# Performance work log

Hardware: AMD Instinct MI355X
Metric: run time of the kernel (lower is better)

## Reference

```python
import jax, jax.numpy as jnp
import numpy as np

B, L, E, H = 1, 2048, 1024, 16
HW = E // H  # head width = 64
SCALE = HW ** -0.5


def setup_inputs() -> dict:
    key = jax.random.key(0)
    ks = jax.random.split(key, 8)
    x = jax.random.normal(ks[0], (B, L, E), dtype=jnp.float32)
    mask = jax.random.bernoulli(ks[1], 0.9, (B, L))
    mask = mask.at[:, 0].set(True)  # guarantee at least one valid key per batch
    bias = jax.random.normal(ks[2], (B, L, L, H), dtype=jnp.float32)
    # torch nn.Linear stores weight as [out, in]; we keep that convention
    w_proj = jax.random.normal(ks[3], (3 * E, E), dtype=jnp.float32) * (E ** -0.5)
    w_o = jax.random.normal(ks[4], (E, E), dtype=jnp.float32) * (E ** -0.5)
    b_o = jax.random.normal(ks[5], (E,), dtype=jnp.float32) * 0.02
    w_g = jax.random.normal(ks[6], (E, E), dtype=jnp.float32) * (E ** -0.5)
    b_g = jax.random.normal(ks[7], (E,), dtype=jnp.float32) * 0.02
    return {"x": x, "mask": mask, "bias": bias, "w_proj": w_proj,
            "w_o": w_o, "b_o": b_o, "w_g": w_g, "b_g": b_g}


def reference(x, mask, bias, w_proj, w_o, b_o, w_g, b_g):
    # proj -> [B, L, 3E], rearrange '(h c)' with h=H so each head slice holds [q|k|v]
    t = jnp.einsum('ble,fe->blf', x, w_proj)               # [B, L, 3E]
    t = t.reshape(B, L, H, 3 * HW).transpose(0, 2, 1, 3)   # [B, H, L, 3*HW]
    q, k, v = jnp.split(t, 3, axis=-1)                     # each [B, H, L, HW]
    a = jnp.einsum('bhqc,bhkc->bhqk', SCALE * q, k)        # [B, H, L, L]
    a = a + bias.transpose(0, 3, 1, 2)                     # bias: [B,Lq,Lk,H] -> [B,H,Lq,Lk]
    a = jnp.where(mask[:, None, None, :], a, -jnp.inf)
    a = jax.nn.softmax(a, axis=-1)
    y = jnp.einsum('bhqk,bhkc->bqhc', a, v).reshape(B, L, E)
    g = jax.nn.sigmoid(jnp.einsum('ble,fe->blf', x, w_g) + b_g)
    y = g * y
    return jnp.einsum('ble,fe->blf', y, w_o) + b_o
```

## Files before the change

kernel.cpp:

```cpp
#include <hip/hip_runtime.h>
#include <stdint.h>

#define LSEQ 2048
#define EMB  1024
#define NH   16
#define HWID 64
#define SCALEF 0.125f

typedef __attribute__((ext_vector_type(4))) float  f32x4;
typedef __attribute__((ext_vector_type(8))) short  bf16x8;
typedef __attribute__((ext_vector_type(8))) unsigned short u16x8;
typedef __attribute__((ext_vector_type(4))) unsigned short u16x4;

static __device__ __forceinline__ unsigned short f2bf(float f) {
    union { float f; unsigned int u; } v; v.f = f;
    unsigned int r = (v.u + 0x7FFFu + ((v.u >> 16) & 1u)) >> 16;
    return (unsigned short)r;
}
static __device__ __forceinline__ float bf2f(unsigned short h) {
    union { unsigned int u; float f; } v; v.u = ((unsigned int)h) << 16;
    return v.f;
}

static __device__ __forceinline__ void gload_lds16(const void* g, void* l) {
    __builtin_amdgcn_global_load_lds((const __attribute__((address_space(1))) void*)g,
                                     (__attribute__((address_space(3))) void*)l,
                                     16, 0, 0);
}

__global__ __launch_bounds__(256) void convert_kernel(
    const float* __restrict__ x, const float* __restrict__ wp,
    const float* __restrict__ wg, const float* __restrict__ wo,
    unsigned short* __restrict__ xb, unsigned short* __restrict__ wcat,
    unsigned short* __restrict__ wob)
{
    const int NX  = (LSEQ * EMB) / 4;
    const int NWP = (3 * EMB * EMB) / 4;
    const int NWG = (EMB * EMB) / 4;
    const int NWO = (EMB * EMB) / 4;
    const int total = NX + NWP + NWG + NWO;
    for (int i = blockIdx.x * blockDim.x + threadIdx.x; i < total;
         i += gridDim.x * blockDim.x) {
        const float4* src; unsigned short* dst; int j;
        if (i < NX)                  { src = (const float4*)x;  dst = xb;                  j = i; }
        else if (i < NX + NWP)       { src = (const float4*)wp; dst = wcat;                j = i - NX; }
        else if (i < NX + NWP + NWG) { src = (const float4*)wg; dst = wcat + 3 * EMB * EMB; j = i - NX - NWP; }
        else                         { src = (const float4*)wo; dst = wob;                 j = i - NX - NWP - NWG; }
        float4 v = src[j];
        u16x4 o;
        o.x = f2bf(v.x); o.y = f2bf(v.y); o.z = f2bf(v.z); o.w = f2bf(v.w);
        *(u16x4*)(dst + (size_t)j * 4) = o;
    }
}

__global__ void decode_mask_kernel(const unsigned char* __restrict__ mask,
                                   unsigned char* __restrict__ valid)
{
    __shared__ int cnt;
    if (threadIdx.x == 0) cnt = 0;
    __syncthreads();
    int c = 0;
    for (int i = threadIdx.x; i < LSEQ; i += 256) c += (mask[i] != 0);
    atomicAdd(&cnt, c);
    __syncthreads();
    bool isbyte = cnt > LSEQ / 2;
    for (int k = threadIdx.x; k < LSEQ; k += 256) {
        unsigned char v;
        if (isbyte) v = (mask[k] != 0);
        else        v = ((mask[4*k] | mask[4*k+1] | mask[4*k+2] | mask[4*k+3]) != 0);
        valid[k] = v;
    }
}

#define BM 128
#define BN 128
#define BK 64

__global__ __launch_bounds__(256) void gemm_bt_kernel(
    const unsigned short* __restrict__ A, const unsigned short* __restrict__ B,
    void* __restrict__ Cout, const float* __restrict__ biasN,
    int M, int N, int K, int epi)
{
    __shared__ unsigned short As[BM][BK];
    __shared__ unsigned short Bs[BN][BK];
    const int tid  = threadIdx.x;
    const int lane = tid & 63;
    const int w    = tid >> 6;
    const int wr   = w >> 1, wc = w & 1;
    const int row0 = blockIdx.y * BM;
    const int col0 = blockIdx.x * BN;
    const int lr = lane & 15;
    const int lg = lane >> 4;

    f32x4 acc[4][4];
    const f32x4 zf = {0.f, 0.f, 0.f, 0.f};
#pragma unroll
    for (int m = 0; m < 4; ++m)
#pragma unroll
        for (int n = 0; n < 4; ++n) acc[m][n] = zf;

    const char* Ab = (const char*)(A + (size_t)row0 * K);
    const char* Bb = (const char*)(B + (size_t)col0 * K);
    const int Kb = K * 2;

    for (int kt = 0; kt < K; kt += BK) {
#pragma unroll
        for (int i = 0; i < 4; ++i) {
            int o = (i * 256 + tid) * 16;
            int r = o >> 7, cb = o & 127;
            gload_lds16(Ab + (size_t)r * Kb + kt * 2 + cb, (char*)As + o);
        }
#pragma unroll
        for (int i = 0; i < 4; ++i) {
            int o = (i * 256 + tid) * 16;
            int r = o >> 7, cb = o & 127;
            gload_lds16(Bb + (size_t)r * Kb + kt * 2 + cb, (char*)Bs + o);
        }
        __syncthreads();
#pragma unroll
        for (int kk = 0; kk < 2; ++kk) {
            bf16x8 af[4], bfr[4];
            const int lk = kk * 32 + lg * 8;
#pragma unroll
            for (int m = 0; m < 4; ++m) af[m]  = *(const bf16x8*)&As[wr * 64 + m * 16 + lr][lk];
#pragma unroll
            for (int n = 0; n < 4; ++n) bfr[n] = *(const bf16x8*)&Bs[wc * 64 + n * 16 + lr][lk];
#pragma unroll
            for (int m = 0; m < 4; ++m)
#pragma unroll
                for (int n = 0; n < 4; ++n)
                    acc[m][n] = __builtin_amdgcn_mfma_f32_16x16x32_bf16(af[m], bfr[n], acc[m][n], 0, 0, 0);
        }
        __syncthreads();
    }

#pragma unroll
    for (int m = 0; m < 4; ++m)
#pragma unroll
        for (int n = 0; n < 4; ++n) {
            const int col = col0 + wc * 64 + n * 16 + lr;
#pragma unroll
            for (int r = 0; r < 4; ++r) {
                const int row = row0 + wr * 64 + m * 16 + lg * 4 + r;
                if (epi == 0)
                    ((unsigned short*)Cout)[(size_t)row * N + col] = f2bf(acc[m][n][r]);
                else
                    ((float*)Cout)[(size_t)row * N + col] = acc[m][n][r] + biasN[col];
            }
        }
}

__global__ __launch_bounds__(256) void rearrange_kernel(
    const unsigned short* __restrict__ T, const float* __restrict__ bg,
    unsigned short* __restrict__ Qh, unsigned short* __restrict__ Kh,
    unsigned short* __restrict__ G)
{
    const int l = blockIdx.x;
    const int t = threadIdx.x;
    const unsigned short* trow = T + (size_t)l * 4096;
    {
        const int tt = t & 127;
        const int h  = tt >> 3;
        const int c0 = (tt & 7) * 8;
        const int srcoff = h * 192 + ((t < 128) ? 0 : 64) + c0;
        u16x8 v = *(const u16x8*)(trow + srcoff);
        unsigned short* dst = ((t < 128) ? Qh : Kh) + ((size_t)h * LSEQ + l) * HWID + c0;
        *(u16x8*)dst = v;
    }
    {
        const int f0 = t * 4;
        float4 b4 = *(const float4*)(bg + f0);
        u16x4 tv = *(const u16x4*)(trow + 3 * EMB + f0);
        u16x4 o;
        o.x = f2bf(1.f / (1.f + __expf(-(bf2f(tv.x) + b4.x))));
        o.y = f2bf(1.f / (1.f + __expf(-(bf2f(tv.y) + b4.y))));
        o.z = f2bf(1.f / (1.f + __expf(-(bf2f(tv.z) + b4.z))));
        o.w = f2bf(1.f / (1.f + __expf(-(bf2f(tv.w) + b4.w))));
        *(u16x4*)(G + (size_t)l * EMB + f0) = o;
    }
}

__global__ __launch_bounds__(256) void vtrans_kernel(
    const unsigned short* __restrict__ T, unsigned short* __restrict__ VT)
{
    __shared__ unsigned short tile[64][72];
    const int h  = blockIdx.x & 15;
    const int lt = blockIdx.x >> 4;
    const int l0 = lt * 64;
    const int t  = threadIdx.x;
    {
        const int i = t >> 2, c0 = (t & 3) * 16;
        const unsigned short* src = T + (size_t)(l0 + i) * 4096 + h * 192 + 128;
        *(u16x8*)&tile[i][c0]     = *(const u16x8*)(src + c0);
        *(u16x8*)&tile[i][c0 + 8] = *(const u16x8*)(src + c0 + 8);
    }
    __syncthreads();
    {
        const int c = t >> 2, j0 = (t & 3) * 16;
        unsigned short* dst = VT + ((size_t)h * HWID + c) * LSEQ + l0 + j0;
        u16x8 a, b;
#pragma unroll
        for (int j = 0; j < 8; ++j) a[j] = tile[j0 + j][c];
#pragma unroll
        for (int j = 0; j < 8; ++j) b[j] = tile[j0 + 8 + j][c];
        *(u16x8*)dst       = a;
        *(u16x8*)(dst + 8) = b;
    }
}

#define KT   32
#define RING 3
#define NT   32
#define SLOT_BYTES (KT * 32 * 16)

__global__ __launch_bounds__(512, 4) void attn_kernel(
    const unsigned short* __restrict__ Qh, const unsigned short* __restrict__ Kh,
    const unsigned short* __restrict__ VT, const float* __restrict__ bias,
    const unsigned char* __restrict__ valid,
    float* __restrict__ Op, float* __restrict__ Ml)
{
    __shared__ char ring[RING * SLOT_BYTES];
    __shared__ unsigned short ps[8][16][40];

    const int tid  = threadIdx.x;
    const int lane = tid & 63;
    const int w    = tid >> 6;
    const int bi = blockIdx.x;
    const int cxl = bi & 7;
    const int hg  = (bi >> 3) & 3;
    const int rr  = bi >> 5;
    const int u   = rr * 8 + cxl;
    const int qt  = u >> 1;
    const int sp  = u & 1;
    const int h    = hg * 4 + (w & 3);
    const int q0b  = qt * 32;
    const int q0w  = q0b + (w >> 2) * 16;
    const int koff = sp * 1024;
    const int lr   = lane & 15;
    const int lg   = lane >> 4;
    const int hloc = w & 3;
    const int qloc = (w >> 2) * 16 + lg * 4;

    const unsigned short* Qbase = Qh + ((size_t)h * LSEQ + q0w) * HWID;
    const bf16x8 qa0 = *(const bf16x8*)(Qbase + lr * HWID + lg * 8);
    const bf16x8 qa1 = *(const bf16x8*)(Qbase + lr * HWID + 32 + lg * 8);

    const unsigned short* Kbase = Kh + (size_t)h * LSEQ * HWID;
    const unsigned short* Vbase = VT + (size_t)h * HWID * LSEQ;
    const char* bias_base = (const char*)bias;

    auto stage = [&](int t) {
        char* dst = ring + (t % RING) * SLOT_BYTES;
        const int kg = koff + t * KT;
#pragma unroll
        for (int p = 0; p < 2; ++p) {
            const int i = p * 512 + tid;
            const int q = i >> 5, k = i & 31;
            gload_lds16(bias_base + ((size_t)(q0b + q) * LSEQ + (kg + k)) * 64 + hg * 16,
                        dst + i * 16);
        }
    };

    float mrow[4], lrow[4];
    f32x4 acc[4];
    const f32x4 zf = {0.f, 0.f, 0.f, 0.f};
#pragma unroll
    for (int r = 0; r < 4; ++r) { mrow[r] = -1e30f; lrow[r] = 0.f; }
#pragma unroll
    for (int c = 0; c < 4; ++c) acc[c] = zf;

    stage(0);
    stage(1);

    for (int t = 0; t < NT; ++t) {
        asm volatile("s_waitcnt vmcnt(2)" ::: "memory");
        __builtin_amdgcn_s_barrier();
        asm volatile("" ::: "memory");

        const int kg = koff + t * KT;
        const float* bs = (const float*)(ring + (t % RING) * SLOT_BYTES);

        const bool v0 = valid[kg + lr] != 0;
        const bool v1 = valid[kg + 16 + lr] != 0;

        f32x4 S[2];
#pragma unroll
        for (int t2 = 0; t2 < 2; ++t2) {
            const unsigned short* kp = Kbase + (size_t)(kg + t2 * 16 + lr) * HWID + lg * 8;
            bf16x8 kb0 = *(const bf16x8*)kp;
            bf16x8 kb1 = *(const bf16x8*)(kp + 32);
            f32x4 s = zf;
            s = __builtin_amdgcn_mfma_f32_16x16x32_bf16(qa0, kb0, s, 0, 0, 0);
            s = __builtin_amdgcn_mfma_f32_16x16x32_bf16(qa1, kb1, s, 0, 0, 0);
            S[t2] = s;
        }

        float sc[2][4], rm[4];
#pragma unroll
        for (int r = 0; r < 4; ++r) {
            const float b0 = bs[(((qloc + r) * 32) + lr) * 4 + hloc];
            const float b1 = bs[(((qloc + r) * 32) + 16 + lr) * 4 + hloc];
            sc[0][r] = v0 ? (S[0][r] * SCALEF + b0) : -1e30f;
            sc[1][r] = v1 ? (S[1][r] * SCALEF + b1) : -1e30f;
            rm[r] = fmaxf(sc[0][r], sc[1][r]);
        }
#pragma unroll
        for (int off = 1; off < 16; off <<= 1)
#pragma unroll
            for (int r = 0; r < 4; ++r)
                rm[r] = fmaxf(rm[r], __shfl_xor(rm[r], off, 64));

        float sf[4], rs[4], p0[4], p1[4];
#pragma unroll
        for (int r = 0; r < 4; ++r) {
            const float mn = fmaxf(mrow[r], rm[r]);
            sf[r] = __expf(mrow[r] - mn);
            mrow[r] = mn;
            p0[r] = v0 ? __expf(sc[0][r] - mn) : 0.f;
            p1[r] = v1 ? __expf(sc[1][r] - mn) : 0.f;
            rs[r] = p0[r] + p1[r];
        }
#pragma unroll
        for (int off = 1; off < 16; off <<= 1)
#pragma unroll
            for (int r = 0; r < 4; ++r)
                rs[r] += __shfl_xor(rs[r], off, 64);
#pragma unroll
        for (int r = 0; r < 4; ++r) lrow[r] = lrow[r] * sf[r] + rs[r];

#pragma unroll
        for (int ct = 0; ct < 4; ++ct)
#pragma unroll
            for (int r = 0; r < 4; ++r) acc[ct][r] *= sf[r];

#pragma unroll
        for (int r = 0; r < 4; ++r) {
            ps[w][lg * 4 + r][lr]      = f2bf(p0[r]);
            ps[w][lg * 4 + r][16 + lr] = f2bf(p1[r]);
        }
        const bf16x8 pa = *(const bf16x8*)&ps[w][lr][lg * 8];

#pragma unroll
        for (int ct = 0; ct < 4; ++ct) {
            bf16x8 vb = *(const bf16x8*)(Vbase + (size_t)(ct * 16 + lr) * LSEQ + kg + lg * 8);
            acc[ct] = __builtin_amdgcn_mfma_f32_16x16x32_bf16(pa, vb, acc[ct], 0, 0, 0);
        }

        if (t + 2 < NT) stage(t + 2);
    }

    const size_t rowb = ((size_t)sp * NH + h) * LSEQ;
#pragma unroll
    for (int ct = 0; ct < 4; ++ct)
#pragma unroll
        for (int r = 0; r < 4; ++r) {
            const int q = q0w + lg * 4 + r;
            Op[(rowb + q) * HWID + ct * 16 + lr] = acc[ct][r];
        }
    if (lr == 0) {
#pragma unroll
        for (int r = 0; r < 4; ++r) {
            const int q = q0w + lg * 4 + r;
            Ml[(rowb + q) * 2 + 0] = mrow[r];
            Ml[(rowb + q) * 2 + 1] = lrow[r];
        }
    }
}

__global__ __launch_bounds__(256) void combine_kernel(
    const float* __restrict__ Op, const float* __restrict__ Ml,
    const unsigned short* __restrict__ G, unsigned short* __restrict__ Yb)
{
    const int t   = threadIdx.x;
    const int c   = t & 63;
    const int row = blockIdx.x * 4 + (t >> 6);
    const int h   = row >> 11;
    const int q   = row & (LSEQ - 1);
    const size_t r0 = (size_t)h * LSEQ + q;
    const size_t r1 = ((size_t)NH + h) * LSEQ + q;
    const float m0 = Ml[r0 * 2 + 0], l0 = Ml[r0 * 2 + 1];
    const float m1 = Ml[r1 * 2 + 0], l1 = Ml[r1 * 2 + 1];
    const float mx = fmaxf(m0, m1);
    const float a0 = __expf(m0 - mx), a1 = __expf(m1 - mx);
    const float inv = 1.f / (l0 * a0 + l1 * a1);
    const float o0 = Op[r0 * HWID + c];
    const float o1 = Op[r1 * HWID + c];
    const float y = (o0 * a0 + o1 * a1) * inv;
    const int e = h * HWID + c;
    const float g = bf2f(G[(size_t)q * EMB + e]);
    Yb[(size_t)q * EMB + e] = f2bf(y * g);
}

extern "C" void kernel_launch(void* const* d_in, const int* in_sizes, int n_in,
                              void* d_out, int out_size, void* d_ws, size_t ws_size,
                              hipStream_t stream) {
    const float*         x      = (const float*)d_in[0];
    const unsigned char* mask   = (const unsigned char*)d_in[1];
    const float*         bias   = (const float*)d_in[2];
    const float*         w_proj = (const float*)d_in[3];
    const float*         w_o    = (const float*)d_in[4];
    const float*         b_o    = (const float*)d_in[5];
    const float*         w_g    = (const float*)d_in[6];
    const float*         b_g    = (const float*)d_in[7];
    float* out = (float*)d_out;
    (void)in_sizes; (void)n_in; (void)out_size; (void)ws_size;

    char* p = (char*)d_ws;
    auto alloc = [&](size_t bytes) {
        char* r = p; p += (bytes + 255) & ~(size_t)255; return r;
    };
    unsigned short* xb    = (unsigned short*)alloc((size_t)LSEQ * EMB * 2);
    unsigned short* wcat  = (unsigned short*)alloc((size_t)4 * EMB * EMB * 2);
    unsigned short* wob   = (unsigned short*)alloc((size_t)EMB * EMB * 2);
    unsigned short* T     = (unsigned short*)alloc((size_t)LSEQ * 4096 * 2);
    unsigned short* Qh    = (unsigned short*)alloc((size_t)NH * LSEQ * HWID * 2);
    unsigned short* Kh    = (unsigned short*)alloc((size_t)NH * LSEQ * HWID * 2);
    unsigned short* VT    = (unsigned short*)alloc((size_t)NH * HWID * LSEQ * 2);
    unsigned short* G     = (unsigned short*)alloc((size_t)LSEQ * EMB * 2);
    unsigned short* Yb    = (unsigned short*)alloc((size_t)LSEQ * EMB * 2);
    unsigned char*  vmask = (unsigned char*)alloc(LSEQ);
    float*          Op    = (float*)alloc((size_t)2 * NH * LSEQ * HWID * 4);
    float*          Ml    = (float*)alloc((size_t)2 * NH * LSEQ * 2 * 4);

    convert_kernel<<<1024, 256, 0, stream>>>(x, w_proj, w_g, w_o, xb, wcat, wob);
    decode_mask_kernel<<<1, 256, 0, stream>>>(mask, vmask);
    gemm_bt_kernel<<<dim3(4096 / BN, LSEQ / BM), 256, 0, stream>>>(
        xb, wcat, (void*)T, nullptr, LSEQ, 4096, EMB, 0);
    rearrange_kernel<<<LSEQ, 256, 0, stream>>>(T, b_g, Qh, Kh, G);
    vtrans_kernel<<<NH * (LSEQ / 64), 256, 0, stream>>>(T, VT);
    attn_kernel<<<512, 512, 0, stream>>>(Qh, Kh, VT, bias, vmask, Op, Ml);
    combine_kernel<<<NH * LSEQ / 4, 256, 0, stream>>>(Op, Ml, G, Yb);
    gemm_bt_kernel<<<dim3(EMB / BN, LSEQ / BM), 256, 0, stream>>>(
        Yb, wob, (void*)out, b_o, LSEQ, EMB, EMB, 1);
}
```

Measured before the change: 267.9 us.

## Load bias directly to registers with prefetch, drop LDS ring and barriers

The attention kernel stops staging the bias tile through a 3-slot LDS ring with barriers. Each lane now loads its own bias values straight from global memory, one iteration ahead in registers, and K/V fragments are loaded at the top of the loop. The Q scaling moves into the rearrange kernel, and the block-index mapping is simplified. The per-lane bias loads are 4-byte strided gathers (stride of 16 heads), which costs coalescing in exchange for removing the barriers and the LDS traffic.

```diff
diff --git a/kernel.cpp b/kernel.cpp
--- a/kernel.cpp
+++ b/kernel.cpp
@@ -162,9 +162,14 @@
         const int tt = t & 127;
         const int h  = tt >> 3;
         const int c0 = (tt & 7) * 8;
-        const int srcoff = h * 192 + ((t < 128) ? 0 : 64) + c0;
+        const bool isq = (t < 128);
+        const int srcoff = h * 192 + (isq ? 0 : 64) + c0;
         u16x8 v = *(const u16x8*)(trow + srcoff);
-        unsigned short* dst = ((t < 128) ? Qh : Kh) + ((size_t)h * LSEQ + l) * HWID + c0;
+        if (isq) {
+#pragma unroll
+            for (int j = 0; j < 8; ++j) v[j] = f2bf(bf2f(v[j]) * SCALEF);
+        }
+        unsigned short* dst = (isq ? Qh : Kh) + ((size_t)h * LSEQ + l) * HWID + c0;
         *(u16x8*)dst = v;
     }
     {
@@ -208,38 +213,27 @@
     }
 }
 
-#define KT   32
-#define RING 3
-#define NT   32
-#define SLOT_BYTES (KT * 32 * 16)
-
 __global__ __launch_bounds__(512, 4) void attn_kernel(
     const unsigned short* __restrict__ Qh, const unsigned short* __restrict__ Kh,
     const unsigned short* __restrict__ VT, const float* __restrict__ bias,
     const unsigned char* __restrict__ valid,
     float* __restrict__ Op, float* __restrict__ Ml)
 {
-    __shared__ char ring[RING * SLOT_BYTES];
     __shared__ unsigned short ps[8][16][40];
 
     const int tid  = threadIdx.x;
     const int lane = tid & 63;
     const int w    = tid >> 6;
     const int bi = blockIdx.x;
-    const int cxl = bi & 7;
-    const int hg  = (bi >> 3) & 3;
-    const int rr  = bi >> 5;
-    const int u   = rr * 8 + cxl;
-    const int qt  = u >> 1;
-    const int sp  = u & 1;
+    const int hg = (bi & 7) >> 1;
+    const int sp = bi & 1;
+    const int qt = bi >> 3;
     const int h    = hg * 4 + (w & 3);
     const int q0b  = qt * 32;
     const int q0w  = q0b + (w >> 2) * 16;
     const int koff = sp * 1024;
     const int lr   = lane & 15;
     const int lg   = lane >> 4;
-    const int hloc = w & 3;
-    const int qloc = (w >> 2) * 16 + lg * 4;
 
     const unsigned short* Qbase = Qh + ((size_t)h * LSEQ + q0w) * HWID;
     const bf16x8 qa0 = *(const bf16x8*)(Qbase + lr * HWID + lg * 8);
@@ -247,19 +241,12 @@
 
     const unsigned short* Kbase = Kh + (size_t)h * LSEQ * HWID;
     const unsigned short* Vbase = VT + (size_t)h * HWID * LSEQ;
-    const char* bias_base = (const char*)bias;
-
-    auto stage = [&](int t) {
-        char* dst = ring + (t % RING) * SLOT_BYTES;
-        const int kg = koff + t * KT;
-#pragma unroll
-        for (int p = 0; p < 2; ++p) {
-            const int i = p * 512 + tid;
-            const int q = i >> 5, k = i & 31;
-            gload_lds16(bias_base + ((size_t)(q0b + q) * LSEQ + (kg + k)) * 64 + hg * 16,
-                        dst + i * 16);
-        }
-    };
+
+    const char* brow[4];
+#pragma unroll
+    for (int r = 0; r < 4; ++r)
+        brow[r] = (const char*)bias +
+                  (((size_t)(q0w + lg * 4 + r) * LSEQ + koff + lr) * NH) * 4 + h * 4;
 
     float mrow[4], lrow[4];
     f32x4 acc[4];
@@ -269,39 +256,53 @@
 #pragma unroll
     for (int c = 0; c < 4; ++c) acc[c] = zf;
 
-    stage(0);
-    stage(1);
-
-    for (int t = 0; t < NT; ++t) {
-        asm volatile("s_waitcnt vmcnt(2)" ::: "memory");
-        __builtin_amdgcn_s_barrier();
-        asm volatile("" ::: "memory");
-
-        const int kg = koff + t * KT;
-        const float* bs = (const float*)(ring + (t % RING) * SLOT_BYTES);
-
+    float bcur[2][4];
+#pragma unroll
+    for (int r = 0; r < 4; ++r) {
+        bcur[0][r] = *(const float*)(brow[r]);
+        bcur[1][r] = *(const float*)(brow[r] + 16 * NH * 4);
+    }
+
+    for (int t = 0; t < 32; ++t) {
+        const int kg = koff + t * 32;
+
+        bf16x8 kb[2][2];
+#pragma unroll
+        for (int t2 = 0; t2 < 2; ++t2) {
+            const unsigned short* kp = Kbase + (size_t)(kg + t2 * 16 + lr) * HWID + lg * 8;
+            kb[t2][0] = *(const bf16x8*)kp;
+            kb[t2][1] = *(const bf16x8*)(kp + 32);
+        }
         const bool v0 = valid[kg + lr] != 0;
         const bool v1 = valid[kg + 16 + lr] != 0;
 
+        bf16x8 vb[4];
+#pragma unroll
+        for (int ct = 0; ct < 4; ++ct)
+            vb[ct] = *(const bf16x8*)(Vbase + (size_t)(ct * 16 + lr) * LSEQ + kg + lg * 8);
+
         f32x4 S[2];
 #pragma unroll
         for (int t2 = 0; t2 < 2; ++t2) {
-            const unsigned short* kp = Kbase + (size_t)(kg + t2 * 16 + lr) * HWID + lg * 8;
-            bf16x8 kb0 = *(const bf16x8*)kp;
-            bf16x8 kb1 = *(const bf16x8*)(kp + 32);
             f32x4 s = zf;
-            s = __builtin_amdgcn_mfma_f32_16x16x32_bf16(qa0, kb0, s, 0, 0, 0);
-            s = __builtin_amdgcn_mfma_f32_16x16x32_bf16(qa1, kb1, s, 0, 0, 0);
+            s = __builtin_amdgcn_mfma_f32_16x16x32_bf16(qa0, kb[t2][0], s, 0, 0, 0);
+            s = __builtin_amdgcn_mfma_f32_16x16x32_bf16(qa1, kb[t2][1], s, 0, 0, 0);
             S[t2] = s;
         }
 
+        const int nk = (t < 31) ? 32 * NH * 4 : 0;
+        float bnxt[2][4];
+#pragma unroll
+        for (int r = 0; r < 4; ++r) {
+            bnxt[0][r] = *(const float*)(brow[r] + nk);
+            bnxt[1][r] = *(const float*)(brow[r] + nk + 16 * NH * 4);
+        }
+
         float sc[2][4], rm[4];
 #pragma unroll
         for (int r = 0; r < 4; ++r) {
-            const float b0 = bs[(((qloc + r) * 32) + lr) * 4 + hloc];
-            const float b1 = bs[(((qloc + r) * 32) + 16 + lr) * 4 + hloc];
-            sc[0][r] = v0 ? (S[0][r] * SCALEF + b0) : -1e30f;
-            sc[1][r] = v1 ? (S[1][r] * SCALEF + b1) : -1e30f;
+            sc[0][r] = v0 ? (S[0][r] + bcur[0][r]) : -1e30f;
+            sc[1][r] = v1 ? (S[1][r] + bcur[1][r]) : -1e30f;
             rm[r] = fmaxf(sc[0][r], sc[1][r]);
         }
 #pragma unroll
@@ -341,12 +342,13 @@
         const bf16x8 pa = *(const bf16x8*)&ps[w][lr][lg * 8];
 
 #pragma unroll
-        for (int ct = 0; ct < 4; ++ct) {
-            bf16x8 vb = *(const bf16x8*)(Vbase + (size_t)(ct * 16 + lr) * LSEQ + kg + lg * 8);
-            acc[ct] = __builtin_amdgcn_mfma_f32_16x16x32_bf16(pa, vb, acc[ct], 0, 0, 0);
-        }
-
-        if (t + 2 < NT) stage(t + 2);
+        for (int ct = 0; ct < 4; ++ct)
+            acc[ct] = __builtin_amdgcn_mfma_f32_16x16x32_bf16(pa, vb[ct], acc[ct], 0, 0, 0);
+
+#pragma unroll
+        for (int r = 0; r < 4; ++r) brow[r] += 32 * NH * 4;
+#pragma unroll
+        for (int r = 0; r < 4; ++r) { bcur[0][r] = bnxt[0][r]; bcur[1][r] = bnxt[1][r]; }
     }
 
     const size_t rowb = ((size_t)sp * NH + h) * LSEQ;
```

Measured after the change: 393.3 us. +46.8%, slower.
